# Kernel optimization log

Hardware: AMD Instinct MI355X
Metric: run time of the kernel (lower is better)

Reference implementation:

```python
import jax, jax.numpy as jnp
import numpy as np

Q_NODES = 100000
S_NODES = 100000
N_EDGES = 3200000
D = 3
HIDDEN = 64
OUT_DIM = 128
STAT_DIM = 3 + 2 * D  # N_i, D_avg, D_var, Delta(D), PCA(D)


def setup_inputs() -> dict:
    key = jax.random.key(0)
    ks = jax.random.split(key, 7)
    source_pos = jax.random.normal(ks[0], (S_NODES, D), dtype=jnp.float32)
    query_pos = jax.random.normal(ks[1], (Q_NODES, D), dtype=jnp.float32)
    qi = jax.random.randint(ks[2], (N_EDGES,), 0, Q_NODES, dtype=jnp.int64)
    si = jax.random.randint(ks[3], (N_EDGES,), 0, S_NODES, dtype=jnp.int64)
    edge_index = jnp.stack([qi, si], axis=0)
    # MLP params (torch Linear default-ish scale)
    W1 = jax.random.normal(ks[4], (HIDDEN, STAT_DIM), dtype=jnp.float32) / np.sqrt(STAT_DIM)
    b1 = jnp.zeros((HIDDEN,), dtype=jnp.float32)
    W2 = jax.random.normal(ks[5], (OUT_DIM, HIDDEN), dtype=jnp.float32) / np.sqrt(HIDDEN)
    b2 = jnp.zeros((OUT_DIM,), dtype=jnp.float32)
    return {"source_pos": source_pos, "query_pos": query_pos, "edge_index": edge_index,
            "W1": W1, "b1": b1, "W2": W2, "b2": b2}


def _stat_features(source_pos, query_pos, edge_index):
    Q = query_pos.shape[0]
    qi = edge_index[0]
    si = edge_index[1]
    ones = jnp.ones(qi.shape, dtype=jnp.float32)
    counts = jax.ops.segment_sum(ones, qi, num_segments=Q)          # [Q] = N_i
    has = counts > 0
    Nc = jnp.where(has, counts, 1.0)                                 # clamp 0 -> 1

    nbr = source_pos[si]                                             # [E,D]
    qc = query_pos[qi]                                               # [E,D]
    dist = jnp.linalg.norm(nbr - qc, axis=1)                         # [E]
    D_avg = jax.ops.segment_sum(dist, qi, num_segments=Q) / Nc       # [Q]
    E_X2 = jax.ops.segment_sum(dist * dist, qi, num_segments=Q) / Nc
    D_var = jnp.maximum(E_X2 - D_avg * D_avg, 0.0)

    centroid = jax.ops.segment_sum(nbr, qi, num_segments=Q) / Nc[:, None]  # [Q,D]
    Delta = centroid - query_pos                                     # [Q,D]

    centered = nbr - centroid[qi]                                    # [E,D]
    cov_comp = centered[:, :, None] * centered[:, None, :]           # [E,D,D]
    cov = jax.ops.segment_sum(cov_comp, qi, num_segments=Q) / Nc[:, None, None]

    eig = jnp.linalg.eigvalsh(cov)[:, ::-1]                          # descending [Q,D]
    PCA = jnp.where(has[:, None], eig, 0.0)

    feats = jnp.concatenate([counts[:, None], D_avg[:, None], D_var[:, None], Delta, PCA], axis=1)
    feats = jnp.where(has[:, None], feats, 0.0)

    mean = feats.mean(axis=0, keepdims=True)
    std = jnp.std(feats, axis=0, ddof=1, keepdims=True)              # torch std is unbiased
    std = jnp.where(std < 1e-6, 1.0, std)
    return (feats - mean) / std


def reference(source_pos, query_pos, edge_index, W1, b1, W2, b2):
    feats = _stat_features(source_pos, query_pos, edge_index)        # [Q, 9]
    h = jax.nn.relu(feats @ W1.T + b1)
    return h @ W2.T + b2                                             # [Q, OUT_DIM]
```

## Files before the change

kernel.cpp:

```cpp
#include <hip/hip_runtime.h>
#include <math.h>

#define Q_NODES 100000
#define S_NODES 100000
#define N_EDGES 3200000
#define HIDDEN 64
#define OUT_DIM 128

#define QPB   128
#define NB    782
#define CAPB  4608
#define TILE  4096
#define NT4   (N_EDGES / 4)

#define F_CURSOR_OFF 0
#define F_NORM_OFF   3200
#define F_PSUM_OFF   3328
#define F_PSUMSQ_OFF 31488
#define F_FEATS_OFF  59648
#define F_SP4_OFF    3659648
#define F_SLOTS_OFF  5259648
#define F_ZERO_BYTES 3200
#define F_WS_NEED    (5259648ull + (unsigned long long)(NB * CAPB + 1) * 4)

#define B_ACC_OFF    0
#define B_STATS_OFF  4800000
#define B_NORM_OFF   4800144
#define B_FEATS_OFF  4800224
#define B_ZERO_BYTES 4800144

__device__ __forceinline__ void atomAddF(float* p, float v) {
#if defined(__gfx950__) || defined(__gfx942__) || defined(__gfx90a__)
    unsafeAtomicAdd(p, v);
#else
    atomicAdd(p, v);
#endif
}


__device__ __forceinline__ void eig3_sym(
        float a00, float a01, float a02, float a11, float a12, float a22,
        float& e1, float& e2, float& e3) {
    float p1 = a01 * a01 + a02 * a02 + a12 * a12;
    float qm = (a00 + a11 + a22) * (1.0f / 3.0f);
    float b00 = a00 - qm, b11 = a11 - qm, b22 = a22 - qm;
    float p2 = b00 * b00 + b11 * b11 + b22 * b22 + 2.0f * p1;
    if (p2 <= 1e-24f) {
        e1 = qm; e2 = qm; e3 = qm;
    } else {
        float p = sqrtf(p2 * (1.0f / 6.0f));
        float invp = 1.0f / p;
        float c00 = b00 * invp, c11 = b11 * invp, c22 = b22 * invp;
        float c01 = a01 * invp, c02 = a02 * invp, c12 = a12 * invp;
        float detB = c00 * (c11 * c22 - c12 * c12)
                   - c01 * (c01 * c22 - c12 * c02)
                   + c02 * (c01 * c12 - c11 * c02);
        float r = 0.5f * detB;
        r = fminf(fmaxf(r, -1.0f), 1.0f);
        float phi = acosf(r) * (1.0f / 3.0f);
        e1 = qm + 2.0f * p * cosf(phi);
        e3 = qm + 2.0f * p * cosf(phi + 2.0943951023931953f);
        e2 = 3.0f * qm - e1 - e3;
    }
}

__device__ __forceinline__ void sums_to_feats(
        const float* s, float qx, float qy, float qz, float* f) {
    float n = s[0];
#pragma unroll
    for (int k = 0; k < 9; ++k) f[k] = 0.0f;
    if (n > 0.0f) {
        float inv = 1.0f / n;
        float Davg = s[1] * inv;
        float Dvar = fmaxf(s[2] * inv - Davg * Davg, 0.0f);
        float cx = s[3] * inv, cy = s[4] * inv, cz = s[5] * inv;
        float a00 = fmaxf(s[6] * inv - cx * cx, 0.0f);
        float a01 = s[7] * inv - cx * cy;
        float a02 = s[8] * inv - cx * cz;
        float a11 = fmaxf(s[9] * inv - cy * cy, 0.0f);
        float a12 = s[10] * inv - cy * cz;
        float a22 = fmaxf(s[11] * inv - cz * cz, 0.0f);
        float e1, e2, e3;
        eig3_sym(a00, a01, a02, a11, a12, a22, e1, e2, e3);
        f[0] = n; f[1] = Davg; f[2] = Dvar;
        f[3] = cx - qx; f[4] = cy - qy; f[5] = cz - qz;
        f[6] = e1; f[7] = e2; f[8] = e3;
    }
}


__global__ __launch_bounds__(256) void pad_kernel(
        const float* __restrict__ sp, float4* __restrict__ sp4) {
    int i = blockIdx.x * 256 + threadIdx.x;
    if (i < S_NODES) sp4[i] = make_float4(sp[3 * i], sp[3 * i + 1], sp[3 * i + 2], 0.0f);
}

__global__ __launch_bounds__(256) void partition_kernel(
        const int* __restrict__ edge,
        int* __restrict__ cursor,
        unsigned int* __restrict__ slots) {
    __shared__ unsigned int s_rec[TILE];
    __shared__ int s_pos[TILE];
    __shared__ int s_hist[NB];
    __shared__ int s_cur[NB];
    __shared__ int s_off[NB];
    __shared__ int s_wsum[4];

    int tid = threadIdx.x;
    int lane = tid & 63, wv = tid >> 6;
    int tileStart = blockIdx.x * TILE;
    int tileCount = N_EDGES - tileStart;
    if (tileCount > TILE) tileCount = TILE;

    for (int b = tid; b < NB; b += 256) s_hist[b] = 0;
    __syncthreads();

    const int4* eq4 = (const int4*)edge;
    const int4* es4 = (const int4*)(edge + N_EDGES);
    int base4 = blockIdx.x * (TILE / 4);
    int4 q4[4], s4[4];
    bool v[4];
#pragma unroll
    for (int j = 0; j < 4; ++j) {
        int i4 = base4 + tid + j * 256;
        v[j] = i4 < NT4;
        int ic = v[j] ? i4 : 0;
        q4[j] = eq4[ic];
        s4[j] = es4[ic];
        if (v[j]) {
            atomicAdd(&s_hist[q4[j].x >> 7], 1);
            atomicAdd(&s_hist[q4[j].y >> 7], 1);
            atomicAdd(&s_hist[q4[j].z >> 7], 1);
            atomicAdd(&s_hist[q4[j].w >> 7], 1);
        }
    }
    __syncthreads();

    int local[4], tsum = 0;
#pragma unroll
    for (int j = 0; j < 4; ++j) {
        int idx = 4 * tid + j;
        local[j] = (idx < NB) ? s_hist[idx] : 0;
        tsum += local[j];
    }
    int inc = tsum;
#pragma unroll
    for (int off = 1; off < 64; off <<= 1) {
        int t = __shfl_up(inc, off);
        if (lane >= off) inc += t;
    }
    if (lane == 63) s_wsum[wv] = inc;
    __syncthreads();
    int wbase = 0;
    for (int w = 0; w < wv; ++w) wbase += s_wsum[w];
    int run = wbase + inc - tsum;
#pragma unroll
    for (int j = 0; j < 4; ++j) {
        int idx = 4 * tid + j;
        if (idx < NB) s_cur[idx] = run;
        run += local[j];
    }
    __syncthreads();

    for (int b = tid; b < NB; b += 256) {
        int c = s_hist[b];
        int base = c ? atomicAdd(&cursor[b], c) : 0;
        s_off[b] = b * CAPB + base - s_cur[b];
    }
    __syncthreads();

#pragma unroll
    for (int j = 0; j < 4; ++j) {
        if (v[j]) {
            int qs[4] = { q4[j].x, q4[j].y, q4[j].z, q4[j].w };
            int ss[4] = { s4[j].x, s4[j].y, s4[j].z, s4[j].w };
#pragma unroll
            for (int m = 0; m < 4; ++m) {
                int bkt = qs[m] >> 7;
                int idx = atomicAdd(&s_cur[bkt], 1);
                int gpos = idx + s_off[bkt];
                if (gpos >= (bkt + 1) * CAPB) gpos = NB * CAPB;
                s_rec[idx] = ((unsigned)(qs[m] & (QPB - 1)) << 17) | (unsigned)ss[m];
                s_pos[idx] = gpos;
            }
        }
    }
    __syncthreads();

    for (int i = tid; i < tileCount; i += 256)
        slots[s_pos[i]] = s_rec[i];
}

__global__ __launch_bounds__(256) void bucket_kernel(
        const int* __restrict__ cursor,
        const unsigned int* __restrict__ slots,
        const float4* __restrict__ sp4,
        const float* __restrict__ qp,
        float* __restrict__ feats,
        float* __restrict__ psum,
        float* __restrict__ psumsq) {
    __shared__ unsigned int s_sorted[CAPB];
    __shared__ float qtile[QPB * 3];
    __shared__ int s_cnt[QPB], s_start[QPB], s_cur[QPB];
    __shared__ float s_red1[4][9], s_red2[4][9];

    int tid = threadIdx.x;
    int b = blockIdx.x;
    int cnt = cursor[b];
    if (cnt > CAPB) cnt = CAPB;

    if (tid < QPB) s_cnt[tid] = 0;
    for (int i = tid; i < QPB * 3; i += 256) {
        int g = b * QPB * 3 + i;
        qtile[i] = (g < Q_NODES * 3) ? qp[g] : 0.0f;
    }
    __syncthreads();

    const unsigned int* bslots = slots + b * CAPB;
    for (int i = tid; i < cnt; i += 256)
        atomicAdd(&s_cnt[bslots[i] >> 17], 1);
    __syncthreads();

    if (tid < 64) {
        int a0 = s_cnt[tid], a1 = s_cnt[64 + tid];
        int i0 = a0, i1 = a1;
#pragma unroll
        for (int off = 1; off < 64; off <<= 1) {
            int t0 = __shfl_up(i0, off); if (tid >= off) i0 += t0;
            int t1 = __shfl_up(i1, off); if (tid >= off) i1 += t1;
        }
        int tot0 = __shfl(i0, 63);
        s_start[tid] = i0 - a0;              s_cur[tid] = i0 - a0;
        s_start[64 + tid] = i1 - a1 + tot0;  s_cur[64 + tid] = i1 - a1 + tot0;
    }
    __syncthreads();

    for (int i = tid; i < cnt; i += 256) {
        unsigned rec = bslots[i];
        int pos = atomicAdd(&s_cur[rec >> 17], 1);
        s_sorted[pos] = rec;
    }
    __syncthreads();

    float f[9];
#pragma unroll
    for (int k = 0; k < 9; ++k) f[k] = 0.0f;
    int q = b * QPB + tid;
    if (tid < QPB && q < Q_NODES) {
        float qx = qtile[3 * tid + 0], qy = qtile[3 * tid + 1], qz = qtile[3 * tid + 2];
        float s[12];
#pragma unroll
        for (int k = 0; k < 12; ++k) s[k] = 0.0f;
        int st = s_start[tid], deg = s_cnt[tid];
        for (int j = 0; j < deg; ++j) {
            unsigned rec = s_sorted[st + j];
            float4 sv = sp4[rec & 0x1FFFF];
            float dx = sv.x - qx, dy = sv.y - qy, dz = sv.z - qz;
            float d2 = dx * dx + dy * dy + dz * dz;
            s[0] += 1.0f;
            s[1] += sqrtf(d2);
            s[2] += d2;
            s[3] += sv.x; s[4] += sv.y; s[5] += sv.z;
            s[6] += sv.x * sv.x; s[7] += sv.x * sv.y; s[8] += sv.x * sv.z;
            s[9] += sv.y * sv.y; s[10] += sv.y * sv.z; s[11] += sv.z * sv.z;
        }
        sums_to_feats(s, qx, qy, qz, f);
#pragma unroll
        for (int k = 0; k < 9; ++k) feats[k * Q_NODES + q] = f[k];
    }

    int lane = tid & 63, wv = tid >> 6;
#pragma unroll
    for (int k = 0; k < 9; ++k) {
        float s1 = f[k];
        float s2 = f[k] * f[k];
#pragma unroll
        for (int off = 32; off > 0; off >>= 1) {
            s1 += __shfl_down(s1, off);
            s2 += __shfl_down(s2, off);
        }
        if (lane == 0) { s_red1[wv][k] = s1; s_red2[wv][k] = s2; }
    }
    __syncthreads();
    if (tid < 9) {
        psum[tid * NB + b]   = s_red1[0][tid] + s_red1[1][tid] + s_red1[2][tid] + s_red1[3][tid];
        psumsq[tid * NB + b] = s_red2[0][tid] + s_red2[1][tid] + s_red2[2][tid] + s_red2[3][tid];
    }
}

__global__ __launch_bounds__(256) void stats_reduce_kernel(
        const float* __restrict__ psum,
        const float* __restrict__ psumsq,
        float* __restrict__ norm) {
    __shared__ double w1[4], w2[4];
    int tid = threadIdx.x, lane = tid & 63, wv = tid >> 6;
    for (int k = 0; k < 9; ++k) {
        double a1 = 0.0, a2 = 0.0;
        for (int b = tid; b < NB; b += 256) {
            a1 += (double)psum[k * NB + b];
            a2 += (double)psumsq[k * NB + b];
        }
#pragma unroll
        for (int off = 32; off > 0; off >>= 1) {
            a1 += __shfl_down(a1, off);
            a2 += __shfl_down(a2, off);
        }
        if (lane == 0) { w1[wv] = a1; w2[wv] = a2; }
        __syncthreads();
        if (tid == 0) {
            double S  = w1[0] + w1[1] + w1[2] + w1[3];
            double S2 = w2[0] + w2[1] + w2[2] + w2[3];
            double mean = S / (double)Q_NODES;
            double var = (S2 - S * S / (double)Q_NODES) / (double)(Q_NODES - 1);
            if (var < 0.0) var = 0.0;
            double sd = sqrt(var);
            if (sd < 1e-6) sd = 1.0;
            norm[k] = (float)mean;
            norm[9 + k] = (float)(1.0 / sd);
        }
        __syncthreads();
    }
}


__global__ __launch_bounds__(256, 3) void mlp_kernel(
        const float* __restrict__ feats,
        const float* __restrict__ norm,
        const float* __restrict__ W1, const float* __restrict__ b1,
        const float* __restrict__ W2, const float* __restrict__ b2,
        float* __restrict__ out) {
    __shared__ float sW1[576];
    __shared__ float sB1[64];
    __shared__ float sB2[64];
    __shared__ float sNorm[18];
    __shared__ float w2t[64 * 64];
    __shared__ float ht[64 * 128];

    int tid = threadIdx.x;
    int blk_q = blockIdx.x >> 1;
    int oh = (blockIdx.x & 1) * 64;

    for (int i = tid; i < 576; i += 256) sW1[i] = W1[i];
    if (tid < 64) { sB1[tid] = b1[tid]; sB2[tid] = b2[oh + tid]; }
    if (tid < 18) sNorm[tid] = norm[tid];
    __syncthreads();

    {
        int o = tid & 63, kc = (tid >> 6) * 16;
#pragma unroll
        for (int j = 0; j < 16; ++j) {
            int k = kc + j;
            w2t[k * 64 + o] = W2[(oh + o) * 64 + k];
        }
    }

    {
        int q = tid & 127, half = tid >> 7;
        int qg = blk_q * 128 + q;
        int qc = qg < Q_NODES ? qg : Q_NODES - 1;
        float f[9];
#pragma unroll
        for (int k = 0; k < 9; ++k)
            f[k] = (feats[k * Q_NODES + qc] - sNorm[k]) * sNorm[9 + k];
#pragma unroll 4
        for (int j = 0; j < 32; ++j) {
            int ko = half * 32 + j;
            float a = sB1[ko];
#pragma unroll
            for (int kf = 0; kf < 9; ++kf) a = fmaf(f[kf], sW1[ko * 9 + kf], a);
            ht[ko * 128 + q] = fmaxf(a, 0.0f);
        }
    }
    __syncthreads();

    int qt = tid >> 4, ot = tid & 15;
    int q0 = qt * 8, o0 = ot * 4;
    float acc[8][4];
#pragma unroll
    for (int i = 0; i < 8; ++i)
#pragma unroll
        for (int j = 0; j < 4; ++j) acc[i][j] = 0.0f;

#pragma unroll 4
    for (int k = 0; k < 64; ++k) {
        float4 h0 = *(const float4*)&ht[k * 128 + q0];
        float4 h1 = *(const float4*)&ht[k * 128 + q0 + 4];
        float4 w  = *(const float4*)&w2t[k * 64 + o0];
        float hh[8] = { h0.x, h0.y, h0.z, h0.w, h1.x, h1.y, h1.z, h1.w };
#pragma unroll
        for (int i = 0; i < 8; ++i) {
            acc[i][0] = fmaf(hh[i], w.x, acc[i][0]);
            acc[i][1] = fmaf(hh[i], w.y, acc[i][1]);
            acc[i][2] = fmaf(hh[i], w.z, acc[i][2]);
            acc[i][3] = fmaf(hh[i], w.w, acc[i][3]);
        }
    }

    float4 bb = *(const float4*)&sB2[o0];
#pragma unroll
    for (int i = 0; i < 8; ++i) {
        int qg = blk_q * 128 + q0 + i;
        if (qg < Q_NODES) {
            float4 v = make_float4(acc[i][0] + bb.x, acc[i][1] + bb.y,
                                   acc[i][2] + bb.z, acc[i][3] + bb.w);
            *(float4*)(out + (size_t)qg * 128 + oh + o0) = v;
        }
    }
}


__global__ __launch_bounds__(256) void edge_kernel(
        const int* __restrict__ edge,
        const float* __restrict__ sp,
        const float* __restrict__ qp,
        float* __restrict__ acc) {
    int e = blockIdx.x * 256 + threadIdx.x;
    if (e >= N_EDGES) return;
    int q = edge[e];
    int s = edge[N_EDGES + e];
    float sx = sp[3 * s + 0], sy = sp[3 * s + 1], sz = sp[3 * s + 2];
    float qx = qp[3 * q + 0], qy = qp[3 * q + 1], qz = qp[3 * q + 2];
    float dx = sx - qx, dy = sy - qy, dz = sz - qz;
    float d2 = dx * dx + dy * dy + dz * dz;
    atomAddF(acc + 0 * Q_NODES + q, 1.0f);
    atomAddF(acc + 1 * Q_NODES + q, sqrtf(d2));
    atomAddF(acc + 2 * Q_NODES + q, d2);
    atomAddF(acc + 3 * Q_NODES + q, sx);
    atomAddF(acc + 4 * Q_NODES + q, sy);
    atomAddF(acc + 5 * Q_NODES + q, sz);
    atomAddF(acc + 6 * Q_NODES + q, sx * sx);
    atomAddF(acc + 7 * Q_NODES + q, sx * sy);
    atomAddF(acc + 8 * Q_NODES + q, sx * sz);
    atomAddF(acc + 9 * Q_NODES + q, sy * sy);
    atomAddF(acc + 10 * Q_NODES + q, sy * sz);
    atomAddF(acc + 11 * Q_NODES + q, sz * sz);
}

__global__ __launch_bounds__(256) void finalize_kernel(
        const float* __restrict__ acc,
        const float* __restrict__ qp,
        float* __restrict__ feats,
        double* __restrict__ stats) {
    int q = blockIdx.x * 256 + threadIdx.x;
    float f[9];
#pragma unroll
    for (int k = 0; k < 9; ++k) f[k] = 0.0f;
    if (q < Q_NODES) {
        float s[12];
#pragma unroll
        for (int k = 0; k < 12; ++k) s[k] = acc[k * Q_NODES + q];
        float qx = qp[3 * q + 0], qy = qp[3 * q + 1], qz = qp[3 * q + 2];
        sums_to_feats(s, qx, qy, qz, f);
#pragma unroll
        for (int k = 0; k < 9; ++k) feats[k * Q_NODES + q] = f[k];
    }
    int lane = threadIdx.x & 63;
#pragma unroll
    for (int k = 0; k < 9; ++k) {
        float s1 = f[k];
        float s2 = f[k] * f[k];
#pragma unroll
        for (int off = 32; off > 0; off >>= 1) {
            s1 += __shfl_down(s1, off);
            s2 += __shfl_down(s2, off);
        }
        if (lane == 0) {
            atomicAdd(&stats[k], (double)s1);
            atomicAdd(&stats[9 + k], (double)s2);
        }
    }
}

__global__ void stats_kernel(const double* __restrict__ stats,
                             float* __restrict__ norm) {
    int k = threadIdx.x;
    if (k < 9) {
        double S = stats[k], S2 = stats[9 + k];
        double mean = S / (double)Q_NODES;
        double var = (S2 - S * S / (double)Q_NODES) / (double)(Q_NODES - 1);
        if (var < 0.0) var = 0.0;
        double sd = sqrt(var);
        if (sd < 1e-6) sd = 1.0;
        norm[k] = (float)mean;
        norm[9 + k] = (float)(1.0 / sd);
    }
}


extern "C" void kernel_launch(void* const* d_in, const int* in_sizes, int n_in,
                              void* d_out, int out_size, void* d_ws, size_t ws_size,
                              hipStream_t stream) {
    const float* sp   = (const float*)d_in[0];
    const float* qp   = (const float*)d_in[1];
    const int*   edge = (const int*)d_in[2];
    const float* W1   = (const float*)d_in[3];
    const float* b1   = (const float*)d_in[4];
    const float* W2   = (const float*)d_in[5];
    const float* b2   = (const float*)d_in[6];
    float* out = (float*)d_out;
    char* ws = (char*)d_ws;

    if (ws_size >= F_WS_NEED) {
        int*          cursor = (int*)(ws + F_CURSOR_OFF);
        float*        norm   = (float*)(ws + F_NORM_OFF);
        float*        psum   = (float*)(ws + F_PSUM_OFF);
        float*        psumsq = (float*)(ws + F_PSUMSQ_OFF);
        float*        feats  = (float*)(ws + F_FEATS_OFF);
        float4*       sp4    = (float4*)(ws + F_SP4_OFF);
        unsigned int* slots  = (unsigned int*)(ws + F_SLOTS_OFF);

        hipMemsetAsync(ws, 0, F_ZERO_BYTES, stream);
        pad_kernel<<<(S_NODES + 255) / 256, 256, 0, stream>>>(sp, sp4);
        partition_kernel<<<(N_EDGES + TILE - 1) / TILE, 256, 0, stream>>>(edge, cursor, slots);
        bucket_kernel<<<NB, 256, 0, stream>>>(cursor, slots, sp4, qp, feats, psum, psumsq);
        stats_reduce_kernel<<<1, 256, 0, stream>>>(psum, psumsq, norm);
        mlp_kernel<<<NB * 2, 256, 0, stream>>>(feats, norm, W1, b1, W2, b2, out);
    } else {
        float*  acc   = (float*)(ws + B_ACC_OFF);
        double* stats = (double*)(ws + B_STATS_OFF);
        float*  norm  = (float*)(ws + B_NORM_OFF);
        float*  feats = (float*)(ws + B_FEATS_OFF);

        hipMemsetAsync(ws, 0, B_ZERO_BYTES, stream);
        edge_kernel<<<N_EDGES / 256, 256, 0, stream>>>(edge, sp, qp, acc);
        finalize_kernel<<<(Q_NODES + 255) / 256, 256, 0, stream>>>(acc, qp, feats, stats);
        stats_kernel<<<1, 64, 0, stream>>>(stats, norm);
        mlp_kernel<<<NB * 2, 256, 0, stream>>>(feats, norm, W1, b1, W2, b2, out);
    }
}
```

Baseline: 204.6 us.

## Fuse padding into partition, widen blocks, split per-query edge loops, merge MLP halves

Several independent changes land together. The source-position padding moves into the partition kernel, and partition and bucket kernels now run 512 threads per block. In the bucket kernel each query's neighbour loop is split across four threads, with partial sums combined through shared memory. The stats reduction gives one wavefront to each feature instead of looping serially, and a single MLP block now computes both 64-wide output halves, so the first layer is no longer computed twice. The aim is fewer launches, better load balance over skewed query degrees and less redundant work, at the cost of more shared memory and extra synchronisation.

```diff
diff --git a/kernel.cpp b/kernel.cpp
--- a/kernel.cpp
+++ b/kernel.cpp
@@ -89,22 +89,17 @@
 }
 
 
-__global__ __launch_bounds__(256) void pad_kernel(
-        const float* __restrict__ sp, float4* __restrict__ sp4) {
-    int i = blockIdx.x * 256 + threadIdx.x;
-    if (i < S_NODES) sp4[i] = make_float4(sp[3 * i], sp[3 * i + 1], sp[3 * i + 2], 0.0f);
-}
-
-__global__ __launch_bounds__(256) void partition_kernel(
+__global__ __launch_bounds__(512, 4) void partition_kernel(
         const int* __restrict__ edge,
+        const float* __restrict__ sp,
+        float4* __restrict__ sp4,
         int* __restrict__ cursor,
         unsigned int* __restrict__ slots) {
     __shared__ unsigned int s_rec[TILE];
-    __shared__ int s_pos[TILE];
-    __shared__ int s_hist[NB];
+    __shared__ int s_posh[TILE];
     __shared__ int s_cur[NB];
     __shared__ int s_off[NB];
-    __shared__ int s_wsum[4];
+    __shared__ int s_wsum[8];
 
     int tid = threadIdx.x;
     int lane = tid & 63, wv = tid >> 6;
@@ -112,26 +107,32 @@
     int tileCount = N_EDGES - tileStart;
     if (tileCount > TILE) tileCount = TILE;
 
-    for (int b = tid; b < NB; b += 256) s_hist[b] = 0;
+    {
+        int i = blockIdx.x * 512 + tid;
+        if (i < S_NODES)
+            sp4[i] = make_float4(sp[3 * i], sp[3 * i + 1], sp[3 * i + 2], 0.0f);
+    }
+
+    for (int b = tid; b < NB; b += 512) s_posh[b] = 0;
     __syncthreads();
 
     const int4* eq4 = (const int4*)edge;
     const int4* es4 = (const int4*)(edge + N_EDGES);
     int base4 = blockIdx.x * (TILE / 4);
-    int4 q4[4], s4[4];
-    bool v[4];
-#pragma unroll
-    for (int j = 0; j < 4; ++j) {
-        int i4 = base4 + tid + j * 256;
+    int4 q4[2], s4[2];
+    bool v[2];
+#pragma unroll
+    for (int j = 0; j < 2; ++j) {
+        int i4 = base4 + tid + j * 512;
         v[j] = i4 < NT4;
         int ic = v[j] ? i4 : 0;
         q4[j] = eq4[ic];
         s4[j] = es4[ic];
         if (v[j]) {
-            atomicAdd(&s_hist[q4[j].x >> 7], 1);
-            atomicAdd(&s_hist[q4[j].y >> 7], 1);
-            atomicAdd(&s_hist[q4[j].z >> 7], 1);
-            atomicAdd(&s_hist[q4[j].w >> 7], 1);
+            atomicAdd(&s_posh[q4[j].x >> 7], 1);
+            atomicAdd(&s_posh[q4[j].y >> 7], 1);
+            atomicAdd(&s_posh[q4[j].z >> 7], 1);
+            atomicAdd(&s_posh[q4[j].w >> 7], 1);
         }
     }
     __syncthreads();
@@ -140,7 +141,7 @@
 #pragma unroll
     for (int j = 0; j < 4; ++j) {
         int idx = 4 * tid + j;
-        local[j] = (idx < NB) ? s_hist[idx] : 0;
+        local[j] = (idx < NB) ? s_posh[idx] : 0;
         tsum += local[j];
     }
     int inc = tsum;
@@ -162,15 +163,15 @@
     }
     __syncthreads();
 
-    for (int b = tid; b < NB; b += 256) {
-        int c = s_hist[b];
+    for (int b = tid; b < NB; b += 512) {
+        int c = s_posh[b];
         int base = c ? atomicAdd(&cursor[b], c) : 0;
         s_off[b] = b * CAPB + base - s_cur[b];
     }
     __syncthreads();
 
 #pragma unroll
-    for (int j = 0; j < 4; ++j) {
+    for (int j = 0; j < 2; ++j) {
         if (v[j]) {
             int qs[4] = { q4[j].x, q4[j].y, q4[j].z, q4[j].w };
             int ss[4] = { s4[j].x, s4[j].y, s4[j].z, s4[j].w };
@@ -181,17 +182,17 @@
                 int gpos = idx + s_off[bkt];
                 if (gpos >= (bkt + 1) * CAPB) gpos = NB * CAPB;
                 s_rec[idx] = ((unsigned)(qs[m] & (QPB - 1)) << 17) | (unsigned)ss[m];
-                s_pos[idx] = gpos;
+                s_posh[idx] = gpos;
             }
         }
     }
     __syncthreads();
 
-    for (int i = tid; i < tileCount; i += 256)
-        slots[s_pos[i]] = s_rec[i];
-}
-
-__global__ __launch_bounds__(256) void bucket_kernel(
+    for (int i = tid; i < tileCount; i += 512)
+        slots[s_posh[i]] = s_rec[i];
+}
+
+__global__ __launch_bounds__(512) void bucket_kernel(
         const int* __restrict__ cursor,
         const unsigned int* __restrict__ slots,
         const float4* __restrict__ sp4,
@@ -202,7 +203,8 @@
     __shared__ unsigned int s_sorted[CAPB];
     __shared__ float qtile[QPB * 3];
     __shared__ int s_cnt[QPB], s_start[QPB], s_cur[QPB];
-    __shared__ float s_red1[4][9], s_red2[4][9];
+    __shared__ float s_part[4][QPB][13];
+    __shared__ float s_red1[8][9], s_red2[8][9];
 
     int tid = threadIdx.x;
     int b = blockIdx.x;
@@ -210,14 +212,14 @@
     if (cnt > CAPB) cnt = CAPB;
 
     if (tid < QPB) s_cnt[tid] = 0;
-    for (int i = tid; i < QPB * 3; i += 256) {
+    for (int i = tid; i < QPB * 3; i += 512) {
         int g = b * QPB * 3 + i;
         qtile[i] = (g < Q_NODES * 3) ? qp[g] : 0.0f;
     }
     __syncthreads();
 
     const unsigned int* bslots = slots + b * CAPB;
-    for (int i = tid; i < cnt; i += 256)
+    for (int i = tid; i < cnt; i += 512)
         atomicAdd(&s_cnt[bslots[i] >> 17], 1);
     __syncthreads();
 
@@ -235,24 +237,22 @@
     }
     __syncthreads();
 
-    for (int i = tid; i < cnt; i += 256) {
+    for (int i = tid; i < cnt; i += 512) {
         unsigned rec = bslots[i];
         int pos = atomicAdd(&s_cur[rec >> 17], 1);
         s_sorted[pos] = rec;
     }
     __syncthreads();
 
-    float f[9];
-#pragma unroll
-    for (int k = 0; k < 9; ++k) f[k] = 0.0f;
-    int q = b * QPB + tid;
-    if (tid < QPB && q < Q_NODES) {
-        float qx = qtile[3 * tid + 0], qy = qtile[3 * tid + 1], qz = qtile[3 * tid + 2];
+    {
+        int q = tid & (QPB - 1);
+        int sub = tid >> 7;
+        float qx = qtile[3 * q + 0], qy = qtile[3 * q + 1], qz = qtile[3 * q + 2];
         float s[12];
 #pragma unroll
         for (int k = 0; k < 12; ++k) s[k] = 0.0f;
-        int st = s_start[tid], deg = s_cnt[tid];
-        for (int j = 0; j < deg; ++j) {
+        int st = s_start[q], deg = s_cnt[q];
+        for (int j = sub; j < deg; j += 4) {
             unsigned rec = s_sorted[st + j];
             float4 sv = sp4[rec & 0x1FFFF];
             float dx = sv.x - qx, dy = sv.y - qy, dz = sv.z - qz;
@@ -264,6 +264,22 @@
             s[6] += sv.x * sv.x; s[7] += sv.x * sv.y; s[8] += sv.x * sv.z;
             s[9] += sv.y * sv.y; s[10] += sv.y * sv.z; s[11] += sv.z * sv.z;
         }
+#pragma unroll
+        for (int k = 0; k < 12; ++k) s_part[sub][q][k] = s[k];
+    }
+    __syncthreads();
+
+    float f[9];
+#pragma unroll
+    for (int k = 0; k < 9; ++k) f[k] = 0.0f;
+    int q = b * QPB + (tid & (QPB - 1));
+    if (tid < QPB && q < Q_NODES) {
+        float qx = qtile[3 * tid + 0], qy = qtile[3 * tid + 1], qz = qtile[3 * tid + 2];
+        float s[12];
+#pragma unroll
+        for (int k = 0; k < 12; ++k)
+            s[k] = ((s_part[0][tid][k] + s_part[1][tid][k])
+                  + (s_part[2][tid][k] + s_part[3][tid][k]));
         sums_to_feats(s, qx, qy, qz, f);
 #pragma unroll
         for (int k = 0; k < 9; ++k) feats[k * Q_NODES + q] = f[k];
@@ -283,42 +299,39 @@
     }
     __syncthreads();
     if (tid < 9) {
-        psum[tid * NB + b]   = s_red1[0][tid] + s_red1[1][tid] + s_red1[2][tid] + s_red1[3][tid];
-        psumsq[tid * NB + b] = s_red2[0][tid] + s_red2[1][tid] + s_red2[2][tid] + s_red2[3][tid];
-    }
-}
-
-__global__ __launch_bounds__(256) void stats_reduce_kernel(
+        float t1 = 0.0f, t2 = 0.0f;
+#pragma unroll
+        for (int w = 0; w < 8; ++w) { t1 += s_red1[w][tid]; t2 += s_red2[w][tid]; }
+        psum[tid * NB + b]   = t1;
+        psumsq[tid * NB + b] = t2;
+    }
+}
+
+__global__ __launch_bounds__(576) void stats_reduce_kernel(
         const float* __restrict__ psum,
         const float* __restrict__ psumsq,
         float* __restrict__ norm) {
-    __shared__ double w1[4], w2[4];
-    int tid = threadIdx.x, lane = tid & 63, wv = tid >> 6;
-    for (int k = 0; k < 9; ++k) {
-        double a1 = 0.0, a2 = 0.0;
-        for (int b = tid; b < NB; b += 256) {
-            a1 += (double)psum[k * NB + b];
-            a2 += (double)psumsq[k * NB + b];
-        }
-#pragma unroll
-        for (int off = 32; off > 0; off >>= 1) {
-            a1 += __shfl_down(a1, off);
-            a2 += __shfl_down(a2, off);
-        }
-        if (lane == 0) { w1[wv] = a1; w2[wv] = a2; }
-        __syncthreads();
-        if (tid == 0) {
-            double S  = w1[0] + w1[1] + w1[2] + w1[3];
-            double S2 = w2[0] + w2[1] + w2[2] + w2[3];
-            double mean = S / (double)Q_NODES;
-            double var = (S2 - S * S / (double)Q_NODES) / (double)(Q_NODES - 1);
-            if (var < 0.0) var = 0.0;
-            double sd = sqrt(var);
-            if (sd < 1e-6) sd = 1.0;
-            norm[k] = (float)mean;
-            norm[9 + k] = (float)(1.0 / sd);
-        }
-        __syncthreads();
+    int k = threadIdx.x >> 6, lane = threadIdx.x & 63;
+    if (k >= 9) return;
+    double a1 = 0.0, a2 = 0.0;
+    for (int b = lane; b < NB; b += 64) {
+        a1 += (double)psum[k * NB + b];
+        a2 += (double)psumsq[k * NB + b];
+    }
+#pragma unroll
+    for (int off = 32; off > 0; off >>= 1) {
+        a1 += __shfl_down(a1, off);
+        a2 += __shfl_down(a2, off);
+    }
+    if (lane == 0) {
+        double S = a1, S2 = a2;
+        double mean = S / (double)Q_NODES;
+        double var = (S2 - S * S / (double)Q_NODES) / (double)(Q_NODES - 1);
+        if (var < 0.0) var = 0.0;
+        double sd = sqrt(var);
+        if (sd < 1e-6) sd = 1.0;
+        norm[k] = (float)mean;
+        norm[9 + k] = (float)(1.0 / sd);
     }
 }
 
@@ -331,28 +344,28 @@
         float* __restrict__ out) {
     __shared__ float sW1[576];
     __shared__ float sB1[64];
-    __shared__ float sB2[64];
+    __shared__ float sB2[128];
     __shared__ float sNorm[18];
     __shared__ float w2t[64 * 64];
     __shared__ float ht[64 * 128];
 
     int tid = threadIdx.x;
-    int blk_q = blockIdx.x >> 1;
-    int oh = (blockIdx.x & 1) * 64;
+    int blk_q = blockIdx.x;
 
     for (int i = tid; i < 576; i += 256) sW1[i] = W1[i];
-    if (tid < 64) { sB1[tid] = b1[tid]; sB2[tid] = b2[oh + tid]; }
+    if (tid < 64) sB1[tid] = b1[tid];
+    if (tid < 128) sB2[tid] = b2[tid];
     if (tid < 18) sNorm[tid] = norm[tid];
-    __syncthreads();
 
     {
         int o = tid & 63, kc = (tid >> 6) * 16;
 #pragma unroll
         for (int j = 0; j < 16; ++j) {
             int k = kc + j;
-            w2t[k * 64 + o] = W2[(oh + o) * 64 + k];
-        }
-    }
+            w2t[k * 64 + o] = W2[o * 64 + k];
+        }
+    }
+    __syncthreads();
 
     {
         int q = tid & 127, half = tid >> 7;
@@ -375,35 +388,51 @@
 
     int qt = tid >> 4, ot = tid & 15;
     int q0 = qt * 8, o0 = ot * 4;
-    float acc[8][4];
-#pragma unroll
-    for (int i = 0; i < 8; ++i)
-#pragma unroll
-        for (int j = 0; j < 4; ++j) acc[i][j] = 0.0f;
+
+#pragma unroll 1
+    for (int pass = 0; pass < 2; ++pass) {
+        int oh = pass * 64;
+        if (pass) {
+            __syncthreads();
+            int o = tid & 63, kc = (tid >> 6) * 16;
+#pragma unroll
+            for (int j = 0; j < 16; ++j) {
+                int k = kc + j;
+                w2t[k * 64 + o] = W2[(oh + o) * 64 + k];
+            }
+            __syncthreads();
+        }
+
+        float acc[8][4];
+#pragma unroll
+        for (int i = 0; i < 8; ++i)
+#pragma unroll
+            for (int j = 0; j < 4; ++j) acc[i][j] = 0.0f;
 
 #pragma unroll 4
-    for (int k = 0; k < 64; ++k) {
-        float4 h0 = *(const float4*)&ht[k * 128 + q0];
-        float4 h1 = *(const float4*)&ht[k * 128 + q0 + 4];
-        float4 w  = *(const float4*)&w2t[k * 64 + o0];
-        float hh[8] = { h0.x, h0.y, h0.z, h0.w, h1.x, h1.y, h1.z, h1.w };
+        for (int k = 0; k < 64; ++k) {
+            float4 h0 = *(const float4*)&ht[k * 128 + q0];
+            float4 h1 = *(const float4*)&ht[k * 128 + q0 + 4];
+            float4 w  = *(const float4*)&w2t[k * 64 + o0];
+            float hh[8] = { h0.x, h0.y, h0.z, h0.w, h1.x, h1.y, h1.z, h1.w };
+#pragma unroll
+            for (int i = 0; i < 8; ++i) {
+                acc[i][0] = fmaf(hh[i], w.x, acc[i][0]);
+                acc[i][1] = fmaf(hh[i], w.y, acc[i][1]);
+                acc[i][2] = fmaf(hh[i], w.z, acc[i][2]);
+                acc[i][3] = fmaf(hh[i], w.w, acc[i][3]);
+            }
+        }
+
+        float4 bb = *(const float4*)&sB2[oh + o0];
 #pragma unroll
         for (int i = 0; i < 8; ++i) {
-            acc[i][0] = fmaf(hh[i], w.x, acc[i][0]);
-            acc[i][1] = fmaf(hh[i], w.y, acc[i][1]);
-            acc[i][2] = fmaf(hh[i], w.z, acc[i][2]);
-            acc[i][3] = fmaf(hh[i], w.w, acc[i][3]);
-        }
-    }
-
-    float4 bb = *(const float4*)&sB2[o0];
-#pragma unroll
-    for (int i = 0; i < 8; ++i) {
-        int qg = blk_q * 128 + q0 + i;
-        if (qg < Q_NODES) {
-            float4 v = make_float4(acc[i][0] + bb.x, acc[i][1] + bb.y,
-                                   acc[i][2] + bb.z, acc[i][3] + bb.w);
-            *(float4*)(out + (size_t)qg * 128 + oh + o0) = v;
+            int qg = blk_q * 128 + q0 + i;
+            if (qg < Q_NODES) {
+                float4 vv = make_float4(acc[i][0] + bb.x, acc[i][1] + bb.y,
+                                        acc[i][2] + bb.z, acc[i][3] + bb.w);
+                *(float4*)(out + (size_t)qg * 128 + oh + o0) = vv;
+            }
         }
     }
 }
@@ -510,11 +539,11 @@
         unsigned int* slots  = (unsigned int*)(ws + F_SLOTS_OFF);
 
         hipMemsetAsync(ws, 0, F_ZERO_BYTES, stream);
-        pad_kernel<<<(S_NODES + 255) / 256, 256, 0, stream>>>(sp, sp4);
-        partition_kernel<<<(N_EDGES + TILE - 1) / TILE, 256, 0, stream>>>(edge, cursor, slots);
-        bucket_kernel<<<NB, 256, 0, stream>>>(cursor, slots, sp4, qp, feats, psum, psumsq);
-        stats_reduce_kernel<<<1, 256, 0, stream>>>(psum, psumsq, norm);
-        mlp_kernel<<<NB * 2, 256, 0, stream>>>(feats, norm, W1, b1, W2, b2, out);
+        partition_kernel<<<(N_EDGES + TILE - 1) / TILE, 512, 0, stream>>>(
+            edge, sp, sp4, cursor, slots);
+        bucket_kernel<<<NB, 512, 0, stream>>>(cursor, slots, sp4, qp, feats, psum, psumsq);
+        stats_reduce_kernel<<<1, 576, 0, stream>>>(psum, psumsq, norm);
+        mlp_kernel<<<NB, 256, 0, stream>>>(feats, norm, W1, b1, W2, b2, out);
     } else {
         float*  acc   = (float*)(ws + B_ACC_OFF);
         double* stats = (double*)(ws + B_STATS_OFF);
@@ -525,6 +554,6 @@
         edge_kernel<<<N_EDGES / 256, 256, 0, stream>>>(edge, sp, qp, acc);
         finalize_kernel<<<(Q_NODES + 255) / 256, 256, 0, stream>>>(acc, qp, feats, stats);
         stats_kernel<<<1, 64, 0, stream>>>(stats, norm);
-        mlp_kernel<<<NB * 2, 256, 0, stream>>>(feats, norm, W1, b1, W2, b2, out);
-    }
-}
+        mlp_kernel<<<NB, 256, 0, stream>>>(feats, norm, W1, b1, W2, b2, out);
+    }
+}
```

Result: faster. 193.1 us (-5.6%).
